# Optimization experiments

Hardware: AMD Instinct MI355X
Metric: run time of the kernel (lower is better)

## Reference

```python
import jax, jax.numpy as jnp
import numpy as np

EPS = 1e-5  # torch BatchNorm1d default eps
N0, N, ORIG, F, K, H, NC = 16, 96, 92, 64, 41, 128, 3


def _bn(x, g, b, axes):
    # training-mode batchnorm: biased batch stats over `axes`, per-channel affine
    m = jnp.mean(x, axis=axes, keepdims=True)
    v = jnp.mean((x - m) ** 2, axis=axes, keepdims=True)
    return (x - m) / jnp.sqrt(v + EPS) * g + b


def setup_inputs() -> dict:
    key = jax.random.key(0)
    ks = jax.random.split(key, 16)
    s = 0.05
    return {
        "atom_fea": jax.random.normal(ks[0], (N0, N, ORIG), jnp.float32),
        "nbr_fea": jax.random.normal(ks[1], (N0, N, N, K), jnp.float32),
        "adj": jax.random.randint(ks[2], (N0, N, N), 0, 2, jnp.int64),
        "emb_W": jax.random.normal(ks[3], (ORIG, F), jnp.float32) * s,
        "emb_b": jnp.zeros((F,), jnp.float32),
        "conv_W": jax.random.normal(ks[4], (NC, 2 * F + K, 2 * F), jnp.float32) * s,
        "conv_b": jnp.zeros((NC, 2 * F), jnp.float32),
        "bn1_g": jnp.ones((NC, 2 * F), jnp.float32),
        "bn1_b": jnp.zeros((NC, 2 * F), jnp.float32),
        "bn2_g": jnp.ones((NC, F), jnp.float32),
        "bn2_b": jnp.zeros((NC, F), jnp.float32),
        "fc_W": jax.random.normal(ks[5], (F, H), jnp.float32) * s,
        "fc_b": jnp.zeros((H,), jnp.float32),
        "out_W": jax.random.normal(ks[6], (H, 1), jnp.float32) * s,
        "out_b": jnp.zeros((1,), jnp.float32),
    }


def reference(atom_fea, nbr_fea, adj, emb_W, emb_b, conv_W, conv_b,
              bn1_g, bn1_b, bn2_g, bn2_b, fc_W, fc_b, out_W, out_b):
    fea = atom_fea @ emb_W + emb_b                       # (N0, N, F)
    adjf = adj.astype(fea.dtype)[..., None]              # (N0, N, N, 1)
    for i in range(NC):
        # NOTE: faithful to source - both FEA and masked term broadcast atom j's
        # own features along the neighbor axis (unsqueeze(2) in torch code).
        FEA = jnp.broadcast_to(fea[:, :, None, :], (N0, N, N, F))
        total = jnp.concatenate([FEA, adjf * FEA, nbr_fea], axis=3)   # (N0,N,N,2F+K)
        gated = total @ conv_W[i] + conv_b[i]                         # (N0,N,N,2F)
        gated = _bn(gated, bn1_g[i], bn1_b[i], (0, 1, 2))
        filt, core = jnp.split(gated, 2, axis=3)
        summed = jnp.sum(jax.nn.sigmoid(filt) * jax.nn.softplus(core), axis=2)  # (N0,N,F)
        summed = _bn(summed, bn2_g[i], bn2_b[i], (0, 1))
        fea = jax.nn.softplus(fea + summed)
    crys = jnp.mean(fea, axis=1)                                      # (N0, F)
    crys = jax.nn.softplus(jax.nn.softplus(crys) @ fc_W + fc_b)       # (N0, H)
    return crys @ out_W + out_b                                       # (N0, 1)
```

## Files before the change

kernel.cpp:

```cpp
#include <hip/hip_runtime.h>
#include <math.h>

#define N0c   16
#define NAt   96
#define ORIG  92
#define Fc    64
#define Kc    41
#define Hc    128
#define NCc   3
#define C2    128
#define EPSBN 1e-5f
#define JG    4
#define JPW   (NAt / JG)
#define NREP  32
#define SRL_STRIDE 12288
#define AROW  72
#define WFRAG 16384
#define INV1  (1.f / (float)(N0c * NAt * NAt))
#define INV2  (1.f / (float)(N0c * NAt))

typedef __attribute__((ext_vector_type(8))) short short8_t;
typedef __attribute__((ext_vector_type(4))) float f32x4;

__device__ __forceinline__ float sp_(float x){
    return fmaxf(x, 0.f) + __logf(1.f + __expf(-fabsf(x)));
}
__device__ __forceinline__ float sgm_(float x){
    return 1.f / (1.f + __expf(-x));
}
__device__ __forceinline__ unsigned short bfhi(float x){
    union { float f; unsigned u; } v; v.f = x;
    unsigned r = v.u + 0x7fff + ((v.u >> 16) & 1);
    return (unsigned short)(r >> 16);
}
__device__ __forceinline__ float bf2f(unsigned short h){
    union { float f; unsigned u; } v; v.u = ((unsigned)h) << 16; return v.f;
}

__global__ __launch_bounds__(256) void k_embed(const float* __restrict__ atom,
                                               const float* __restrict__ W,
                                               const float* __restrict__ b,
                                               float* __restrict__ fea){
    int row = blockIdx.x * 4 + (threadIdx.x >> 6);
    int f   = threadIdx.x & 63;
    const float* ar = atom + row * ORIG;
    float acc = b[f];
    #pragma unroll 4
    for (int o = 0; o < ORIG; ++o) acc += ar[o] * W[o * Fc + f];
    fea[row * Fc + f] = acc;
}

__global__ __launch_bounds__(256) void k_pre(const float* __restrict__ nbr,
                                             const int*   __restrict__ adj,
                                             float* __restrict__ ST,
                                             float* __restrict__ cntf){
    int r    = blockIdx.x;
    int lane = threadIdx.x & 63;
    int jg   = __builtin_amdgcn_readfirstlane(threadIdx.x >> 6);
    __shared__ float rS[JG][Kc], rT[JG][Kc], rc[JG];
    float S = 0.f, T = 0.f, cn = 0.f;
    int j0 = jg * JPW;
    for (int j = j0; j < j0 + JPW; ++j){
        float a = (float)adj[r * NAt + j];
        float v = (lane < Kc) ? nbr[((size_t)r * NAt + j) * Kc + lane] : 0.f;
        S += v; T += a * v; cn += a;
    }
    if (lane < Kc){ rS[jg][lane] = S; rT[jg][lane] = T; }
    if (lane == 0) rc[jg] = cn;
    __syncthreads();
    int t = threadIdx.x;
    if (t < Kc){
        ST[r * (2 * Kc) + t]      = rS[0][t] + rS[1][t] + rS[2][t] + rS[3][t];
        ST[r * (2 * Kc) + Kc + t] = rT[0][t] + rT[1][t] + rT[2][t] + rT[3][t];
    }
    if (t == 0) cntf[r] = rc[0] + rc[1] + rc[2] + rc[3];
}

__global__ __launch_bounds__(128) void k_gram(const float* __restrict__ nbr,
                                              float* __restrict__ pG, int rpb){
    int blk = blockIdx.x;
    int t   = threadIdx.x;
    int k   = (t % 21) * 2;
    int lb  = (t / 21) * 7;
    __shared__ float L[NAt * Kc];
    float a0[7] = {0,0,0,0,0,0,0}, a1[7] = {0,0,0,0,0,0,0};
    for (int rr = 0; rr < rpb; ++rr){
        int r = blk * rpb + rr;
        __syncthreads();
        for (int i = t; i < NAt * Kc; i += 128)
            L[i] = nbr[(size_t)r * NAt * Kc + i];
        __syncthreads();
        if (t < 126){
            for (int j = 0; j < NAt; ++j){
                float vk0 = L[j * Kc + k];
                float vk1 = (k + 1 < Kc) ? L[j * Kc + k + 1] : 0.f;
                #pragma unroll
                for (int m = 0; m < 7; ++m){
                    if (lb + m < Kc){
                        float lv = L[j * Kc + lb + m];
                        a0[m] += vk0 * lv;
                        a1[m] += vk1 * lv;
                    }
                }
            }
        }
    }
    if (t < 126){
        float* dst = pG + (size_t)blk * (Kc * Kc);
        #pragma unroll
        for (int m = 0; m < 7; ++m){
            if (lb + m < Kc){
                dst[k * Kc + lb + m] = a0[m];
                if (k + 1 < Kc) dst[(k + 1) * Kc + lb + m] = a1[m];
            }
        }
    }
}

__global__ __launch_bounds__(64) void k_gred(const float* __restrict__ pG,
                                             float* __restrict__ G){
    int i  = (blockIdx.x % 27) * 64 + threadIdx.x;
    int b0 = (blockIdx.x / 27) * 96;
    if (i < Kc * Kc){
        float s = 0.f;
        #pragma unroll 4
        for (int b = b0; b < b0 + 96; ++b) s += pG[(size_t)b * (Kc * Kc) + i];
        atomicAdd(&G[i], s);
    }
}

__global__ void k_wt(const float* __restrict__ convW, float* __restrict__ W3T){
    int l = blockIdx.x, c = threadIdx.x;
    const float* Wl = convW + (size_t)l * 169 * C2;
    float* dst = W3T + ((size_t)l * C2 + c) * 44;
    for (int k = 0; k < Kc; ++k) dst[k] = Wl[(C2 + k) * C2 + c];
    dst[41] = 0.f; dst[42] = 0.f; dst[43] = 0.f;
}

__global__ __launch_bounds__(256) void k_wtb(const float* __restrict__ convW,
                                             unsigned short* __restrict__ W3F){
    int l = blockIdx.x;
    const float* Wl = convW + (size_t)l * 169 * C2;
    for (int it = 0; it < 8; ++it){
        int idx  = threadIdx.x + it * 256;
        int lane = idx & 63;
        int fid  = idx >> 6;
        int h    = fid & 1;
        int ks   = (fid >> 1) & 1;
        int nt   = fid >> 2;
        int n    = nt * 16 + (lane & 15);
        unsigned short* dst = W3F + (size_t)l * WFRAG + fid * 512 + lane * 8;
        #pragma unroll
        for (int i = 0; i < 8; ++i){
            int k = ks * 32 + (lane >> 4) * 8 + i;
            float w = (k < Kc) ? Wl[(C2 + k) * C2 + n] : 0.f;
            unsigned short hi = bfhi(w);
            dst[i] = h ? bfhi(w - bf2f(hi)) : hi;
        }
    }
}

__global__ __launch_bounds__(128) void k_quad(const float* __restrict__ G,
                                              const float* __restrict__ convW,
                                              float* __restrict__ q3){
    int l = blockIdx.x, c = threadIdx.x;
    const float* Wl = convW + (size_t)l * 169 * C2;
    __shared__ float GL[Kc * Kc];
    for (int i = c; i < Kc * Kc; i += 128) GL[i] = G[i];
    float w3[Kc];
    #pragma unroll
    for (int k = 0; k < Kc; ++k) w3[k] = Wl[(C2 + k) * C2 + c];
    __syncthreads();
    float q = 0.f;
    for (int k = 0; k < Kc; ++k){
        float gw = 0.f;
        #pragma unroll
        for (int m = 0; m < Kc; ++m) gw += GL[k * Kc + m] * w3[m];
        q += w3[k] * gw;
    }
    q3[l * C2 + c] = q;
}

__global__ __launch_bounds__(256)
void k_front(float* __restrict__ fea,
             const float* __restrict__ Wl,
             const float* __restrict__ bl,
             const float* __restrict__ W3Tl,
             const float* __restrict__ ST,
             const float* __restrict__ cntf,
             float* __restrict__ p1,
             float* __restrict__ p2,
             float* __restrict__ sum1R,
             float* __restrict__ sq1R,
             const float* __restrict__ summed,
             const float* __restrict__ sum2Rp,
             const float* __restrict__ sq2Rp,
             const float* __restrict__ g2p,
             const float* __restrict__ b2p,
             int upd){
    int r    = blockIdx.x;
    int tid  = threadIdx.x;
    int c    = tid & 127;
    int half = __builtin_amdgcn_readfirstlane(tid >> 7);
    __shared__ float F[Fc];
    __shared__ float A2L[Fc], B2L[Fc];
    __shared__ float P1h[C2], P2h[C2], TTs[C2];

    if (upd){
        if (tid < Fc){
            float s = 0.f, q = 0.f;
            for (int rr = 0; rr < NREP; ++rr){
                s += sum2Rp[rr * Fc + tid];
                q += sq2Rp[rr * Fc + tid];
            }
            float m = s * INV2;
            float v = q * INV2 - m * m;
            float A = g2p[tid] * rsqrtf(v + EPSBN);
            A2L[tid] = A;
            B2L[tid] = b2p[tid] - m * A;
        }
        __syncthreads();
        if (tid < Fc){
            float nv = sp_(fea[r * Fc + tid] + summed[r * Fc + tid] * A2L[tid] + B2L[tid]);
            F[tid] = nv;
            fea[r * Fc + tid] = nv;
        }
        __syncthreads();
    } else {
        if (tid < Fc) F[tid] = fea[r * Fc + tid];
        __syncthreads();
    }

    float a1p = 0.f, a2p = 0.f;
    int f0 = half * 32;
    #pragma unroll 8
    for (int f = f0; f < f0 + 32; ++f){
        float fv = F[f];
        a1p += fv * Wl[f * C2 + c];
        a2p += fv * Wl[(Fc + f) * C2 + c];
    }
    const float* wt = W3Tl + c * 44;
    const float* Sr = ST + r * (2 * Kc) + half * Kc;
    float dot = 0.f;
    #pragma unroll
    for (int k = 0; k < 40; k += 4){
        float4 wv = *(const float4*)(wt + k);
        dot += Sr[k] * wv.x + Sr[k + 1] * wv.y + Sr[k + 2] * wv.z + Sr[k + 3] * wv.w;
    }
    dot += Sr[40] * wt[40];

    if (half == 1){ P1h[c] = a1p; P2h[c] = a2p; TTs[c] = dot; }
    __syncthreads();
    if (half == 0){
        float a1 = a1p + P1h[c] + bl[c];
        float a2 = a2p + P2h[c];
        float u  = dot;
        float tt = TTs[c];
        p1[r * C2 + c] = a1;
        p2[r * C2 + c] = a2;
        float cn = cntf[r];
        float s1 = (float)NAt * a1 + cn * a2 + u;
        float q1 = (float)NAt * a1 * a1 + cn * a2 * a2
                 + 2.f * cn * a1 * a2 + 2.f * a1 * u + 2.f * a2 * tt;
        int slot = blockIdx.x & (NREP - 1);
        atomicAdd(&sum1R[slot * C2 + c], s1);
        atomicAdd(&sq1R[slot * C2 + c], q1);
    }
}

__global__ __launch_bounds__(512)
void k_apply(const float* __restrict__ nbr,
             const int*   __restrict__ adj,
             const unsigned short* __restrict__ W3Fl,
             const float* __restrict__ p1,
             const float* __restrict__ p2,
             const float* __restrict__ sum1R,
             const float* __restrict__ sq1R,
             const float* __restrict__ qv,
             const float* __restrict__ g1,
             const float* __restrict__ b1,
             float* __restrict__ summed,
             float* __restrict__ sum2R,
             float* __restrict__ sq2R){
    int r    = blockIdx.x;
    int tid  = threadIdx.x;
    int lane = tid & 63;
    int w    = __builtin_amdgcn_readfirstlane(tid >> 6);
    int ntF  = w & 3;
    int mh   = w >> 2;

    __shared__ unsigned short sAH[NAt * AROW];
    __shared__ unsigned short sAL[NAt * AROW];
    __shared__ float AJ[NAt];
    __shared__ float PL1[C2], PL2[C2], A1L[C2], B1L[C2];
    __shared__ float TpW[8][16];

    short8_t BH[2][2], BL[2][2];
    #pragma unroll
    for (int ni = 0; ni < 2; ++ni){
        int nt = ntF + ni * 4;
        #pragma unroll
        for (int ks = 0; ks < 2; ++ks){
            int fidH = (nt * 2 + ks) * 2;
            BH[ni][ks] = *(const short8_t*)(W3Fl + fidH * 512 + lane * 8);
            BL[ni][ks] = *(const short8_t*)(W3Fl + (fidH + 1) * 512 + lane * 8);
        }
    }

    const float* nb = nbr + (size_t)r * (NAt * Kc);
    for (int idx = tid; idx < NAt * Kc; idx += 512){
        int j = idx / Kc, k = idx - j * Kc;
        float x = nb[idx];
        unsigned short hi = bfhi(x);
        sAH[j * AROW + k] = hi;
        sAL[j * AROW + k] = bfhi(x - bf2f(hi));
    }
    for (int idx = tid; idx < NAt * 23; idx += 512){
        int j = idx / 23, k = Kc + (idx - j * 23);
        sAH[j * AROW + k] = 0;
        sAL[j * AROW + k] = 0;
    }
    if (tid < C2){
        int c = tid;
        float s = 0.f, q = 0.f;
        for (int rr = 0; rr < NREP; ++rr){ s += sum1R[rr * C2 + c]; q += sq1R[rr * C2 + c]; }
        float m = s * INV1;
        float v = (q + qv[c]) * INV1 - m * m;
        float A = g1[c] * rsqrtf(v + EPSBN);
        A1L[c] = A;
        B1L[c] = b1[c] - m * A;
    } else if (tid < 256){
        PL1[tid - 128] = p1[r * C2 + tid - 128];
    } else if (tid < 384){
        PL2[tid - 256] = p2[r * C2 + tid - 256];
    } else if (tid < 480){
        AJ[tid - 384] = (float)adj[r * NAt + tid - 384];
    }
    __syncthreads();

    f32x4 acc[3][2] = {};
    int q4 = (lane >> 4) * 8;
    #pragma unroll
    for (int mt = 0; mt < 3; ++mt){
        int jrow = (mh * 48 + mt * 16 + (lane & 15)) * AROW;
        short8_t AH0 = *(const short8_t*)(&sAH[jrow + q4]);
        short8_t AH1 = *(const short8_t*)(&sAH[jrow + 32 + q4]);
        short8_t AL0 = *(const short8_t*)(&sAL[jrow + q4]);
        short8_t AL1 = *(const short8_t*)(&sAL[jrow + 32 + q4]);
        #pragma unroll
        for (int ni = 0; ni < 2; ++ni){
            acc[mt][ni] = __builtin_amdgcn_mfma_f32_16x16x32_bf16(AH0, BH[ni][0], acc[mt][ni], 0, 0, 0);
            acc[mt][ni] = __builtin_amdgcn_mfma_f32_16x16x32_bf16(AH0, BL[ni][0], acc[mt][ni], 0, 0, 0);
            acc[mt][ni] = __builtin_amdgcn_mfma_f32_16x16x32_bf16(AL0, BH[ni][0], acc[mt][ni], 0, 0, 0);
            acc[mt][ni] = __builtin_amdgcn_mfma_f32_16x16x32_bf16(AH1, BH[ni][1], acc[mt][ni], 0, 0, 0);
            acc[mt][ni] = __builtin_amdgcn_mfma_f32_16x16x32_bf16(AH1, BL[ni][1], acc[mt][ni], 0, 0, 0);
            acc[mt][ni] = __builtin_amdgcn_mfma_f32_16x16x32_bf16(AL1, BH[ni][1], acc[mt][ni], 0, 0, 0);
        }
    }

    int cF = ntF * 16 + (lane & 15);
    int cC = cF + 64;
    float p1F = PL1[cF], p2F = PL2[cF], A1F = A1L[cF], B1F = B1L[cF];
    float p1C = PL1[cC], p2C = PL2[cC], A1C = A1L[cC], B1C = B1L[cC];
    float tsum = 0.f;
    #pragma unroll
    for (int mt = 0; mt < 3; ++mt){
        #pragma unroll
        for (int rg = 0; rg < 4; ++rg){
            int j = mh * 48 + mt * 16 + (lane >> 4) * 4 + rg;
            float ajf = AJ[j];
            float gf = (p1F + ajf * p2F + acc[mt][0][rg]) * A1F + B1F;
            float gc = (p1C + ajf * p2C + acc[mt][1][rg]) * A1C + B1C;
            tsum += sgm_(gf) * sp_(gc);
        }
    }
    tsum += __shfl_xor(tsum, 16);
    tsum += __shfl_xor(tsum, 32);
    if (lane < 16) TpW[w][lane] = tsum;
    __syncthreads();
    if (tid < Fc){
        int f = tid;
        float s = TpW[f >> 4][f & 15] + TpW[(f >> 4) + 4][f & 15];
        summed[r * Fc + f] = s;
        int slot = blockIdx.x & (NREP - 1);
        atomicAdd(&sum2R[slot * Fc + f], s);
        atomicAdd(&sq2R[slot * Fc + f], s * s);
    }
}

__global__ __launch_bounds__(128) void k_final(const float* __restrict__ fea,
                                               const float* __restrict__ summed,
                                               const float* __restrict__ sum2R,
                                               const float* __restrict__ sq2R,
                                               const float* __restrict__ g2,
                                               const float* __restrict__ b2,
                                               const float* __restrict__ fcW,
                                               const float* __restrict__ fcb,
                                               const float* __restrict__ outW,
                                               const float* __restrict__ outb,
                                               float* __restrict__ out){
    int b = blockIdx.x;
    int t = threadIdx.x;
    __shared__ float spc[Fc];
    __shared__ float red[Hc];
    if (t < Fc){
        float s = 0.f, q = 0.f;
        for (int r = 0; r < NREP; ++r){ s += sum2R[r * Fc + t]; q += sq2R[r * Fc + t]; }
        float m  = s * INV2;
        float v  = q * INV2 - m * m;
        float A2 = g2[t] * rsqrtf(v + EPSBN);
        float B2 = b2[t] - m * A2;
        float acc = 0.f;
        for (int i = 0; i < NAt; ++i){
            int idx = (b * NAt + i) * Fc + t;
            acc += sp_(fea[idx] + summed[idx] * A2 + B2);
        }
        spc[t] = sp_(acc * (1.f / NAt));
    }
    __syncthreads();
    float h = fcb[t];
    #pragma unroll 4
    for (int f = 0; f < Fc; ++f) h += spc[f] * fcW[f * Hc + t];
    h = sp_(h);
    red[t] = h * outW[t];
    __syncthreads();
    for (int off = 64; off > 0; off >>= 1){
        if (t < off) red[t] += red[t + off];
        __syncthreads();
    }
    if (t == 0) out[b] = red[0] + outb[0];
}

extern "C" void kernel_launch(void* const* d_in, const int* in_sizes, int n_in,
                              void* d_out, int out_size, void* d_ws, size_t ws_size,
                              hipStream_t stream){
    const float* atom  = (const float*)d_in[0];
    const float* nbr   = (const float*)d_in[1];
    const int*   adj   = (const int*)  d_in[2];
    const float* embW  = (const float*)d_in[3];
    const float* embB  = (const float*)d_in[4];
    const float* convW = (const float*)d_in[5];
    const float* convB = (const float*)d_in[6];
    const float* bn1g  = (const float*)d_in[7];
    const float* bn1b  = (const float*)d_in[8];
    const float* bn2g  = (const float*)d_in[9];
    const float* bn2b  = (const float*)d_in[10];
    const float* fcW   = (const float*)d_in[11];
    const float* fcb   = (const float*)d_in[12];
    const float* outW  = (const float*)d_in[13];
    const float* outb  = (const float*)d_in[14];
    float* out = (float*)d_out;
    float* ws  = (float*)d_ws;

    const int ROWS = N0c * NAt;
    float* fea    = ws;
    float* p1     = ws + 98304;
    float* p2     = ws + 294912;
    float* summed = ws + 491520;
    float* SRL    = ws + 589824;
    float* ST     = ws + 626688;
    float* cntf   = ws + 752640;
    float* q3     = ws + 754176;
    float* W3T    = ws + 754560;
    unsigned short* W3F = (unsigned short*)(ws + 771456);
    const size_t PERS = 796032;

    size_t ws_f = ws_size / sizeof(float);
    int nblk; float *pG, *G;
    if (ws_f >= PERS + (size_t)1536 * 1681 + 1681 + 64){
        nblk = 1536; pG = ws + PERS; G = pG + (size_t)nblk * 1681;
    } else if (ws_f >= PERS + (size_t)768 * 1681 + 1681 + 64){
        nblk = 768;  pG = ws + PERS; G = pG + (size_t)nblk * 1681;
    } else if (ws_f >= PERS + (size_t)384 * 1681 + 1681 + 64){
        nblk = 384;  pG = ws + PERS; G = pG + (size_t)nblk * 1681;
    } else {
        nblk = 384;  pG = ws;        G = ws + 650000;
    }
    int rpb = 1536 / nblk;
    int ph  = nblk / 96;

    hipMemsetAsync(G, 0, Kc * Kc * sizeof(float), stream);
    k_gram <<<nblk, 128, 0, stream>>>(nbr, pG, rpb);
    k_gred <<<27 * ph, 64, 0, stream>>>(pG, G);
    k_wt   <<<NCc, C2, 0, stream>>>(convW, W3T);
    k_wtb  <<<NCc, 256, 0, stream>>>(convW, W3F);
    k_quad <<<NCc, C2, 0, stream>>>(G, convW, q3);
    k_embed<<<ROWS / 4, 256, 0, stream>>>(atom, embW, embB, fea);
    k_pre  <<<ROWS, 256, 0, stream>>>(nbr, adj, ST, cntf);
    hipMemsetAsync(SRL, 0, 3 * SRL_STRIDE * sizeof(float), stream);

    for (int l = 0; l < NCc; ++l){
        const float* Wl   = convW + (size_t)l * 169 * C2;
        const float* bl   = convB + l * C2;
        const float* W3Tl = W3T + (size_t)l * C2 * 44;
        const unsigned short* W3Fl = W3F + (size_t)l * WFRAG;
        float* sum1R = SRL + l * SRL_STRIDE;
        float* sq1R  = sum1R + 4096;
        float* sum2R = sum1R + 8192;
        float* sq2R  = sum1R + 10240;
        const float* sum2Rp = (l > 0) ? SRL + (l - 1) * SRL_STRIDE + 8192 : SRL;
        const float* sq2Rp  = (l > 0) ? SRL + (l - 1) * SRL_STRIDE + 10240 : SRL;
        const float* g2p    = bn2g + (l > 0 ? (l - 1) : 0) * Fc;
        const float* b2p    = bn2b + (l > 0 ? (l - 1) : 0) * Fc;

        k_front <<<ROWS, 256, 0, stream>>>(fea, Wl, bl, W3Tl, ST, cntf,
                                           p1, p2, sum1R, sq1R,
                                           summed, sum2Rp, sq2Rp, g2p, b2p,
                                           l > 0 ? 1 : 0);
        k_apply <<<ROWS, 512, 0, stream>>>(nbr, adj, W3Fl, p1, p2,
                                           sum1R, sq1R, q3 + l * C2,
                                           bn1g + l * C2, bn1b + l * C2,
                                           summed, sum2R, sq2R);
    }

    k_final<<<N0c, Hc, 0, stream>>>(fea, summed,
                                    SRL + 2 * SRL_STRIDE + 8192,
                                    SRL + 2 * SRL_STRIDE + 10240,
                                    bn2g + 2 * Fc, bn2b + 2 * Fc,
                                    fcW, fcb, outW, outb, out);
}
```

Measured before the change: 294.0 us.

## Fuse preprocessing kernels: ST stats into gram, embed into front, weight prep merged

The per-row neighbor sums (S, T) and adjacency counts are now computed inside k_gram from the nbr tile it already holds in shared memory. This removes the separate k_pre pass that re-read the full nbr tensor; k_pre now runs only in the compact-workspace fallback. The embedding matmul moves into the first k_front call, and k_wt, k_wtb and k_quad become a single k_prep kernel. The G memset is replaced by block 0 of k_gram zeroing G. Together these cut several launches and one large global read, at the cost of extra serial work in a few gram threads.

Measured after the change: 287.4 us. 1.02x faster.

```diff
diff --git a/kernel.cpp b/kernel.cpp
--- a/kernel.cpp
+++ b/kernel.cpp
@@ -37,19 +37,6 @@
     union { float f; unsigned u; } v; v.u = ((unsigned)h) << 16; return v.f;
 }
 
-__global__ __launch_bounds__(256) void k_embed(const float* __restrict__ atom,
-                                               const float* __restrict__ W,
-                                               const float* __restrict__ b,
-                                               float* __restrict__ fea){
-    int row = blockIdx.x * 4 + (threadIdx.x >> 6);
-    int f   = threadIdx.x & 63;
-    const float* ar = atom + row * ORIG;
-    float acc = b[f];
-    #pragma unroll 4
-    for (int o = 0; o < ORIG; ++o) acc += ar[o] * W[o * Fc + f];
-    fea[row * Fc + f] = acc;
-}
-
 __global__ __launch_bounds__(256) void k_pre(const float* __restrict__ nbr,
                                              const int*   __restrict__ adj,
                                              float* __restrict__ ST,
@@ -77,19 +64,43 @@
 }
 
 __global__ __launch_bounds__(128) void k_gram(const float* __restrict__ nbr,
-                                              float* __restrict__ pG, int rpb){
+                                              const int*   __restrict__ adj,
+                                              float* __restrict__ pG,
+                                              float* __restrict__ ST,
+                                              float* __restrict__ cntf,
+                                              float* __restrict__ G,
+                                              int rpb, int doST){
     int blk = blockIdx.x;
     int t   = threadIdx.x;
     int k   = (t % 21) * 2;
     int lb  = (t / 21) * 7;
     __shared__ float L[NAt * Kc];
+    __shared__ float AJf[NAt];
+    if (blk == 0){
+        for (int i = t; i < Kc * Kc; i += 128) G[i] = 0.f;
+    }
     float a0[7] = {0,0,0,0,0,0,0}, a1[7] = {0,0,0,0,0,0,0};
     for (int rr = 0; rr < rpb; ++rr){
         int r = blk * rpb + rr;
         __syncthreads();
         for (int i = t; i < NAt * Kc; i += 128)
             L[i] = nbr[(size_t)r * NAt * Kc + i];
+        if (t < NAt) AJf[t] = (float)adj[r * NAt + t];
         __syncthreads();
+        if (doST && t < Kc){
+            float S = 0.f, T = 0.f;
+            for (int j = 0; j < NAt; ++j){
+                float v = L[j * Kc + t];
+                S += v; T += AJf[j] * v;
+            }
+            ST[r * (2 * Kc) + t]      = S;
+            ST[r * (2 * Kc) + Kc + t] = T;
+        }
+        if (doST && t == Kc){
+            float cn = 0.f;
+            for (int j = 0; j < NAt; ++j) cn += AJf[j];
+            cntf[r] = cn;
+        }
         if (t < 126){
             for (int j = 0; j < NAt; ++j){
                 float vk0 = L[j * Kc + k];
@@ -129,20 +140,19 @@
     }
 }
 
-__global__ void k_wt(const float* __restrict__ convW, float* __restrict__ W3T){
-    int l = blockIdx.x, c = threadIdx.x;
+__global__ __launch_bounds__(256) void k_prep(const float* __restrict__ G,
+                                              const float* __restrict__ convW,
+                                              float* __restrict__ W3T,
+                                              unsigned short* __restrict__ W3F,
+                                              float* __restrict__ q3){
+    int l   = blockIdx.x;
+    int tid = threadIdx.x;
     const float* Wl = convW + (size_t)l * 169 * C2;
-    float* dst = W3T + ((size_t)l * C2 + c) * 44;
-    for (int k = 0; k < Kc; ++k) dst[k] = Wl[(C2 + k) * C2 + c];
-    dst[41] = 0.f; dst[42] = 0.f; dst[43] = 0.f;
-}
-
-__global__ __launch_bounds__(256) void k_wtb(const float* __restrict__ convW,
-                                             unsigned short* __restrict__ W3F){
-    int l = blockIdx.x;
-    const float* Wl = convW + (size_t)l * 169 * C2;
+    __shared__ float GL[Kc * Kc];
+    for (int i = tid; i < Kc * Kc; i += 256) GL[i] = G[i];
+    __syncthreads();
     for (int it = 0; it < 8; ++it){
-        int idx  = threadIdx.x + it * 256;
+        int idx  = tid + it * 256;
         int lane = idx & 63;
         int fid  = idx >> 6;
         int h    = fid & 1;
@@ -152,37 +162,38 @@
         unsigned short* dst = W3F + (size_t)l * WFRAG + fid * 512 + lane * 8;
         #pragma unroll
         for (int i = 0; i < 8; ++i){
-            int k = ks * 32 + (lane >> 4) * 8 + i;
-            float w = (k < Kc) ? Wl[(C2 + k) * C2 + n] : 0.f;
+            int kk = ks * 32 + (lane >> 4) * 8 + i;
+            float w = (kk < Kc) ? Wl[(C2 + kk) * C2 + n] : 0.f;
             unsigned short hi = bfhi(w);
             dst[i] = h ? bfhi(w - bf2f(hi)) : hi;
         }
     }
-}
-
-__global__ __launch_bounds__(128) void k_quad(const float* __restrict__ G,
-                                              const float* __restrict__ convW,
-                                              float* __restrict__ q3){
-    int l = blockIdx.x, c = threadIdx.x;
-    const float* Wl = convW + (size_t)l * 169 * C2;
-    __shared__ float GL[Kc * Kc];
-    for (int i = c; i < Kc * Kc; i += 128) GL[i] = G[i];
-    float w3[Kc];
-    #pragma unroll
-    for (int k = 0; k < Kc; ++k) w3[k] = Wl[(C2 + k) * C2 + c];
-    __syncthreads();
-    float q = 0.f;
-    for (int k = 0; k < Kc; ++k){
-        float gw = 0.f;
+    if (tid < C2){
+        int c = tid;
+        float* dstT = W3T + ((size_t)l * C2 + c) * 44;
+        float w3[Kc];
         #pragma unroll
-        for (int m = 0; m < Kc; ++m) gw += GL[k * Kc + m] * w3[m];
-        q += w3[k] * gw;
-    }
-    q3[l * C2 + c] = q;
+        for (int kk = 0; kk < Kc; ++kk){
+            w3[kk] = Wl[(C2 + kk) * C2 + c];
+            dstT[kk] = w3[kk];
+        }
+        dstT[41] = 0.f; dstT[42] = 0.f; dstT[43] = 0.f;
+        float q = 0.f;
+        for (int kk = 0; kk < Kc; ++kk){
+            float gw = 0.f;
+            #pragma unroll
+            for (int m = 0; m < Kc; ++m) gw += GL[kk * Kc + m] * w3[m];
+            q += w3[kk] * gw;
+        }
+        q3[l * C2 + c] = q;
+    }
 }
 
 __global__ __launch_bounds__(256)
 void k_front(float* __restrict__ fea,
+             const float* __restrict__ atom,
+             const float* __restrict__ embW,
+             const float* __restrict__ embB,
              const float* __restrict__ Wl,
              const float* __restrict__ bl,
              const float* __restrict__ W3Tl,
@@ -227,7 +238,14 @@
         }
         __syncthreads();
     } else {
-        if (tid < Fc) F[tid] = fea[r * Fc + tid];
+        if (tid < Fc){
+            const float* ar = atom + r * ORIG;
+            float acc = embB[tid];
+            #pragma unroll 4
+            for (int o = 0; o < ORIG; ++o) acc += ar[o] * embW[o * Fc + tid];
+            F[tid] = acc;
+            fea[r * Fc + tid] = acc;
+        }
         __syncthreads();
     }
 
@@ -466,7 +484,7 @@
     const size_t PERS = 796032;
 
     size_t ws_f = ws_size / sizeof(float);
-    int nblk; float *pG, *G;
+    int nblk; float *pG, *G; int compact = 0;
     if (ws_f >= PERS + (size_t)1536 * 1681 + 1681 + 64){
         nblk = 1536; pG = ws + PERS; G = pG + (size_t)nblk * 1681;
     } else if (ws_f >= PERS + (size_t)768 * 1681 + 1681 + 64){
@@ -474,19 +492,17 @@
     } else if (ws_f >= PERS + (size_t)384 * 1681 + 1681 + 64){
         nblk = 384;  pG = ws + PERS; G = pG + (size_t)nblk * 1681;
     } else {
-        nblk = 384;  pG = ws;        G = ws + 650000;
+        nblk = 384;  pG = ws;        G = ws + 650000;  compact = 1;
     }
     int rpb = 1536 / nblk;
     int ph  = nblk / 96;
 
-    hipMemsetAsync(G, 0, Kc * Kc * sizeof(float), stream);
-    k_gram <<<nblk, 128, 0, stream>>>(nbr, pG, rpb);
+    k_gram <<<nblk, 128, 0, stream>>>(nbr, adj, pG, ST, cntf, G, rpb,
+                                      compact ? 0 : 1);
     k_gred <<<27 * ph, 64, 0, stream>>>(pG, G);
-    k_wt   <<<NCc, C2, 0, stream>>>(convW, W3T);
-    k_wtb  <<<NCc, 256, 0, stream>>>(convW, W3F);
-    k_quad <<<NCc, C2, 0, stream>>>(G, convW, q3);
-    k_embed<<<ROWS / 4, 256, 0, stream>>>(atom, embW, embB, fea);
-    k_pre  <<<ROWS, 256, 0, stream>>>(nbr, adj, ST, cntf);
+    k_prep <<<NCc, 256, 0, stream>>>(G, convW, W3T, W3F, q3);
+    if (compact)
+        k_pre <<<ROWS, 256, 0, stream>>>(nbr, adj, ST, cntf);
     hipMemsetAsync(SRL, 0, 3 * SRL_STRIDE * sizeof(float), stream);
 
     for (int l = 0; l < NCc; ++l){
@@ -503,7 +519,8 @@
         const float* g2p    = bn2g + (l > 0 ? (l - 1) : 0) * Fc;
         const float* b2p    = bn2b + (l > 0 ? (l - 1) : 0) * Fc;
 
-        k_front <<<ROWS, 256, 0, stream>>>(fea, Wl, bl, W3Tl, ST, cntf,
+        k_front <<<ROWS, 256, 0, stream>>>(fea, atom, embW, embB,
+                                           Wl, bl, W3Tl, ST, cntf,
                                            p1, p2, sum1R, sq1R,
                                            summed, sum2Rp, sq2Rp, g2p, b2p,
                                            l > 0 ? 1 : 0);
```
